# Performance work log

Measured on AMD Instinct MI355X. Metric: run time of the kernel, lower is better.

The kernel has to match this reference:

```python
import jax, jax.numpy as jnp
import numpy as np

B = 10      # number of interacting objects
NDIM = 2    # self.n: position/velocity dimensionality

# Edge list equivalent to rel_rec/rel_send one-hot matrices (edges grouped by receiver)
_rec_idx, _send_idx = np.where(~np.eye(B, dtype=bool))


def _mlp(x, W0, b0, W1, b1, W2, b2):
    # MLP with 2 hidden softplus layers, linear output
    h = jax.nn.softplus(x @ W0 + b0)
    h = jax.nn.softplus(h @ W1 + b1)
    return h @ W2 + b2


def setup_inputs() -> dict:
    key = jax.random.key(0)
    ks = jax.random.split(key, 7)
    N = 8192            # trajectories per batch
    H = 128             # hidden width of self-dynamics MLP
    Hi = 128            # hidden width of interaction MLP
    nin = 2 * NDIM      # self MLP input dim (pos+vel)
    nout = 2 * NDIM     # n_f_out for order=1
    nin_i = 3 * NDIM    # interaction MLP input dim (p1-p2, v1, v2)
    w = lambda k, shp: jax.random.normal(k, shp, jnp.float32) / np.float32(np.sqrt(shp[0]))
    return {
        "z": jax.random.normal(ks[0], (N * B, 2 * NDIM), jnp.float32),
        "fW0": w(ks[1], (nin, H)),   "fb0": jnp.zeros((H,), jnp.float32),
        "fW1": w(ks[2], (H, H)),     "fb1": jnp.zeros((H,), jnp.float32),
        "fW2": w(ks[3], (H, nout)),  "fb2": jnp.zeros((nout,), jnp.float32),
        "iW0": w(ks[4], (nin_i, Hi)),"ib0": jnp.zeros((Hi,), jnp.float32),
        "iW1": w(ks[5], (Hi, Hi)),   "ib1": jnp.zeros((Hi,), jnp.float32),
        "iW2": w(ks[6], (Hi, nout)), "ib2": jnp.zeros((nout,), jnp.float32),
    }


def reference(z, fW0, fb0, fW1, fb1, fW2, fb2, iW0, ib0, iW1, ib1, iW2, ib2):
    # One evaluation of the ODE vector field (order=1, n_aug_dyn=n_aug_st=0).
    n = NDIM
    NB = z.shape[0]
    N = NB // B
    dz_self = _mlp(z, fW0, fb0, fW1, fb1, fW2, fb2)            # [N*B, 2n]
    z3 = z.reshape(N, B, 2 * n)
    recv = z3[:, _rec_idx]                                     # [N, B(B-1), 2n] gather (node2edge)
    send = z3[:, _send_idx]
    # odefint input: (p_recv - p_send, v_recv, v_send)  -> [N, B(B-1), 3n]
    inp = jnp.concatenate([recv[..., :n] - send[..., :n], recv[..., n:], send[..., n:]], -1)
    dz_int = _mlp(inp, iW0, ib0, iW1, ib1, iW2, ib2)           # [N, B(B-1), 2n]
    dz_int = dz_int.reshape(N, B, B - 1, 2 * n).sum(2)         # sum over senders per receiver
    dz = dz_self.reshape(N, B, 2 * n) + dz_int
    return dz.reshape(NB, 2 * n)
```

## Files before the change

kernel.cpp:

```cpp
#include <hip/hip_runtime.h>
#include <hip/hip_bf16.h>

#define NDIM 2
#define BB 10
#define H 128
#define PAIRS 90
#define MROWS 128
#define LDH 136
#define USLD 132
#define LOG2E 1.4426950408889634f

typedef short short8 __attribute__((ext_vector_type(8)));
typedef float floatx4 __attribute__((ext_vector_type(4)));
typedef float floatx16 __attribute__((ext_vector_type(16)));

__device__ inline short f2bf(float x) {
    unsigned u = __float_as_uint(x);
    return (short)((u + 0x7fffu + ((u >> 16) & 1u)) >> 16);
}

#if __has_builtin(__builtin_amdgcn_cvt_pk_bf16_f32)
typedef __bf16 bf16x2_t __attribute__((ext_vector_type(2)));
__device__ inline unsigned pk2(float a, float b) {
    bf16x2_t v = __builtin_amdgcn_cvt_pk_bf16_f32(a, b);
    return __builtin_bit_cast(unsigned, v);
}
#else
__device__ inline unsigned pk2(float a, float b) {
    unsigned ua = __float_as_uint(a), ub = __float_as_uint(b);
    ua = (ua + 0x7fffu + ((ua >> 16) & 1u)) >> 16;
    ub = (ub + 0x7fffu + ((ub >> 16) & 1u)) & 0xffff0000u;
    return ua | ub;
}
#endif

__device__ inline float sp2(float xs) {
#if __has_builtin(__builtin_amdgcn_exp2f) && __has_builtin(__builtin_amdgcn_logf)
    float t = __builtin_amdgcn_exp2f(xs);
    return __builtin_amdgcn_logf(1.f + t) * 0.6931471805599453f;
#else
    return log2f(1.f + exp2f(xs)) * 0.6931471805599453f;
#endif
}

__global__ void prep_weights(const float* __restrict__ iW1, const float* __restrict__ fW1,
                             const float* __restrict__ iW2, const float* __restrict__ fW2,
                             const float* __restrict__ ib1, const float* __restrict__ fb1,
                             const float* __restrict__ iW0, const float* __restrict__ ib0,
                             const float* __restrict__ fW0, const float* __restrict__ fb0,
                             short* __restrict__ W1Fi, short* __restrict__ W1Ff,
                             short* __restrict__ W2Fi, short* __restrict__ W2Ff,
                             float* __restrict__ scal) {
    int t = blockIdx.x * blockDim.x + threadIdx.x;
    int stride = gridDim.x * blockDim.x;
    for (int fidx = t; fidx < 16384; fidx += stride) {
        int j = fidx & 7, lane = (fidx >> 3) & 63, nt = (fidx >> 9) & 3, ks = fidx >> 11;
        int k = 16 * ks + ((lane >> 5) << 3) + j;
        int n = 32 * nt + (lane & 31);
        W1Fi[fidx] = f2bf(iW1[k * H + n] * LOG2E);
        W1Ff[fidx] = f2bf(fW1[k * H + n] * LOG2E);
    }
    for (int fidx = t; fidx < 2048; fidx += stride) {
        int j = fidx & 7, lane = (fidx >> 3) & 63, ks = fidx >> 9;
        int k = 32 * ks + ((lane >> 4) << 3) + j;
        int n = lane & 15;
        W2Fi[fidx] = (n < 4) ? f2bf(iW2[k * 4 + n]) : (short)0;
        W2Ff[fidx] = (n < 4) ? f2bf(fW2[k * 4 + n]) : (short)0;
    }
    if (t < 128) {
        scal[t] = ib1[t] * LOG2E;
        scal[128 + t] = fb1[t] * LOG2E;
        scal[1024 + t] = ib0[t] * LOG2E;
        scal[1664 + t] = fb0[t] * LOG2E;
    }
    if (t < 768) scal[256 + t] = iW0[t] * LOG2E;
    if (t < 512) scal[1152 + t] = fW0[t] * LOG2E;
}

__global__ __launch_bounds__(512, 6) void fused_kernel(
    const float* __restrict__ z,
    const float* __restrict__ ib2, const float* __restrict__ fb2,
    const short* __restrict__ W1Fi, const short* __restrict__ W2Fi,
    const short* __restrict__ W1Ff, const short* __restrict__ W2Ff,
    const float* __restrict__ scal, float* __restrict__ out) {
    __shared__ __align__(16) short h0s[MROWS * LDH];
    __shared__ __align__(16) float uws[2 * BB * USLD];
    __shared__ __align__(16) float4 zs4[BB];
    float* us   = uws;
    float* wss  = uws + BB * USLD;
    float* outs = uws;

    int n = blockIdx.x;
    int tid = threadIdx.x, lane = tid & 63, wave = tid >> 6;
    int c31 = lane & 31, halfk = lane >> 5;
    int ntw = wave & 3, mhalf = wave >> 2;

    short8 af[8];
#pragma unroll
    for (int ks = 0; ks < 8; ++ks)
        af[ks] = *(const short8*)(W1Fi + ((ks * 4 + ntw) * 64 + lane) * 8);

    if (tid < BB) zs4[tid] = ((const float4*)z)[n * BB + tid];
    __syncthreads();

    {
        int c = tid & 127;
        const float* iW0s = scal + 256;
        float w0 = iW0s[c], w1 = iW0s[128 + c], w2 = iW0s[256 + c];
        float w3 = iW0s[384 + c], w4 = iW0s[512 + c], w5 = iW0s[640 + c];
        float b0v = scal[1024 + c];
        int bb0 = tid >> 7;
#pragma unroll
        for (int t = 0; t < 3; ++t) {
            int b = bb0 + 4 * t;
            if (b < BB) {
                float4 zb = zs4[b];
                us[b * USLD + c]  = b0v + zb.x * w0 + zb.y * w1 + zb.z * w2 + zb.w * w3;
                wss[b * USLD + c] = -zb.x * w0 - zb.y * w1 + zb.z * w4 + zb.w * w5;
            }
        }
    }
    if (tid < 320) {
        int b = tid >> 5, c4 = (tid & 31) * 4;
        const float* fW0s = scal + 1152;
        float4 zb = zs4[b];
        float4 q0 = *(const float4*)(fW0s + c4);
        float4 q1 = *(const float4*)(fW0s + 128 + c4);
        float4 q2 = *(const float4*)(fW0s + 256 + c4);
        float4 q3 = *(const float4*)(fW0s + 384 + c4);
        float4 qb = *(const float4*)(scal + 1664 + c4);
        float a0 = qb.x + zb.x * q0.x + zb.y * q1.x + zb.z * q2.x + zb.w * q3.x;
        float a1 = qb.y + zb.x * q0.y + zb.y * q1.y + zb.z * q2.y + zb.w * q3.y;
        float a2 = qb.z + zb.x * q0.z + zb.y * q1.z + zb.z * q2.z + zb.w * q3.z;
        float a3 = qb.w + zb.x * q0.w + zb.y * q1.w + zb.z * q2.w + zb.w * q3.w;
        uint2 pk;
        pk.x = pk2(sp2(a0), sp2(a1));
        pk.y = pk2(sp2(a2), sp2(a3));
        *(uint2*)(h0s + (96 + b) * LDH + c4) = pk;
    }
    if (tid < 352) {
        int r = 106 + (tid >> 4), kk8 = (tid & 15) * 8;
        *(uint4*)(h0s + r * LDH + kk8) = uint4{0u, 0u, 0u, 0u};
    }
    __syncthreads();

    {
        int m0 = tid >> 4, kk8 = (tid & 15) * 8;
#pragma unroll
        for (int t = 0; t < 3; ++t) {
            int m = m0 + 32 * t;
            uint4 pk = {0u, 0u, 0u, 0u};
            if (m < PAIRS) {
                int i = (m * 57) >> 9;
                int s = m - 9 * i;
                int j = s + (s >= i);
                float4 ua = *(float4*)(us + i * USLD + kk8);
                float4 ub = *(float4*)(us + i * USLD + kk8 + 4);
                float4 wa = *(float4*)(wss + j * USLD + kk8);
                float4 wb = *(float4*)(wss + j * USLD + kk8 + 4);
                pk.x = pk2(sp2(ua.x + wa.x), sp2(ua.y + wa.y));
                pk.y = pk2(sp2(ua.z + wa.z), sp2(ua.w + wa.w));
                pk.z = pk2(sp2(ub.x + wb.x), sp2(ub.y + wb.y));
                pk.w = pk2(sp2(ub.z + wb.z), sp2(ub.w + wb.w));
            }
            *(uint4*)(h0s + m * LDH + kk8) = pk;
        }
    }
    __syncthreads();

    int hb = 32 * ntw + 4 * halfk;
    floatx16 acc0, acc1;
    {
        const float* blo = scal;
        const float* bhi = mhalf ? (scal + 128) : scal;
#pragma unroll
        for (int g = 0; g < 4; ++g) {
            float4 v0 = *(const float4*)(blo + hb + 8 * g);
            float4 v1 = *(const float4*)(bhi + hb + 8 * g);
            acc0[4 * g + 0] = v0.x; acc0[4 * g + 1] = v0.y;
            acc0[4 * g + 2] = v0.z; acc0[4 * g + 3] = v0.w;
            acc1[4 * g + 0] = v1.x; acc1[4 * g + 1] = v1.y;
            acc1[4 * g + 2] = v1.z; acc1[4 * g + 3] = v1.w;
        }
    }
    int rowA = 64 * mhalf + c31;
    int rowB = rowA + 32;
#pragma unroll
    for (int ks = 0; ks < 8; ++ks) {
        short8 bf = *(const short8*)(h0s + rowA * LDH + 16 * ks + 8 * halfk);
        acc0 = __builtin_amdgcn_mfma_f32_32x32x16_bf16(af[ks], bf, acc0, 0, 0, 0);
    }
    if (mhalf) {
#pragma unroll
        for (int ks = 0; ks < 8; ++ks)
            af[ks] = *(const short8*)(W1Ff + ((ks * 4 + ntw) * 64 + lane) * 8);
    }
#pragma unroll
    for (int ks = 0; ks < 8; ++ks) {
        short8 bf = *(const short8*)(h0s + rowB * LDH + 16 * ks + 8 * halfk);
        acc1 = __builtin_amdgcn_mfma_f32_32x32x16_bf16(af[ks], bf, acc1, 0, 0, 0);
    }
    __syncthreads();

#pragma unroll
    for (int g = 0; g < 4; ++g) {
        uint2 pa, pb;
        pa.x = pk2(sp2(acc0[4 * g + 0]), sp2(acc0[4 * g + 1]));
        pa.y = pk2(sp2(acc0[4 * g + 2]), sp2(acc0[4 * g + 3]));
        pb.x = pk2(sp2(acc1[4 * g + 0]), sp2(acc1[4 * g + 1]));
        pb.y = pk2(sp2(acc1[4 * g + 2]), sp2(acc1[4 * g + 3]));
        *(uint2*)(h0s + rowA * LDH + 32 * ntw + 8 * g + 4 * halfk) = pa;
        *(uint2*)(h0s + rowB * LDH + 32 * ntw + 8 * g + 4 * halfk) = pb;
    }
    __syncthreads();

    {
        int rit = lane & 15, quad = lane >> 4;
        if (wave < 7) {
            const short* W2 = (wave == 6) ? W2Ff : W2Fi;
            const float* b2 = (wave == 6) ? fb2 : ib2;
            short8 w2v[4];
#pragma unroll
            for (int ks = 0; ks < 4; ++ks)
                w2v[ks] = *(const short8*)(W2 + (ks * 64 + lane) * 8);
            floatx4 a = {0.f, 0.f, 0.f, 0.f};
            if (quad == 0) {
                float4 bbv = *(const float4*)b2;
                a = floatx4{bbv.x, bbv.y, bbv.z, bbv.w};
            }
#pragma unroll
            for (int ks = 0; ks < 4; ++ks) {
                short8 bf = *(const short8*)(h0s + (16 * wave + rit) * LDH + 32 * ks + quad * 8);
                a = __builtin_amdgcn_mfma_f32_16x16x32_bf16(w2v[ks], bf, a, 0, 0, 0);
            }
            if (quad == 0) {
                float4 o = {a[0], a[1], a[2], a[3]};
                *(float4*)(outs + (16 * wave + rit) * 4) = o;
            }
        }
    }
    __syncthreads();

    if (tid < BB * 4) {
        int i = tid >> 2, c = tid & 3;
        float s = outs[(96 + i) * 4 + c];
#pragma unroll
        for (int p = 0; p < 9; ++p) s += outs[(9 * i + p) * 4 + c];
        out[(n * BB + i) * 4 + c] = s;
    }
}

extern "C" void kernel_launch(void* const* d_in, const int* in_sizes, int n_in,
                              void* d_out, int out_size, void* d_ws, size_t ws_size,
                              hipStream_t stream) {
    const float* z   = (const float*)d_in[0];
    const float* fW0 = (const float*)d_in[1];
    const float* fb0 = (const float*)d_in[2];
    const float* fW1 = (const float*)d_in[3];
    const float* fb1 = (const float*)d_in[4];
    const float* fW2 = (const float*)d_in[5];
    const float* fb2 = (const float*)d_in[6];
    const float* iW0 = (const float*)d_in[7];
    const float* ib0 = (const float*)d_in[8];
    const float* iW1 = (const float*)d_in[9];
    const float* ib1 = (const float*)d_in[10];
    const float* iW2 = (const float*)d_in[11];
    const float* ib2 = (const float*)d_in[12];
    float* out = (float*)d_out;

    short* wsS = (short*)d_ws;
    short* W1Fi = wsS;
    short* W1Ff = wsS + 16384;
    short* W2Fi = wsS + 32768;
    short* W2Ff = wsS + 34816;
    float* scal = (float*)(wsS + 36864);

    int NB = in_sizes[0] / (2 * NDIM);
    int Nsys = NB / BB;

    hipLaunchKernelGGL(prep_weights, dim3(128), dim3(256), 0, stream,
                       iW1, fW1, iW2, fW2, ib1, fb1, iW0, ib0, fW0, fb0,
                       W1Fi, W1Ff, W2Fi, W2Ff, scal);
    hipLaunchKernelGGL(fused_kernel, dim3(Nsys), dim3(512), 0, stream,
                       z, ib2, fb2, W1Fi, W2Fi, W1Ff, W2Ff, scal, out);
}
```

Before: 181.8 us.

## Cut registers and LDS: bf16 edge partials, polynomial softplus, streamed weight fragments

Several changes aimed at raising occupancy and trimming per-element cost. Launch bounds go from 6 to 8 waves per SIMD. Layer-1 weight fragments are streamed one k-step ahead instead of holding eight in registers, and the second-layer weights are loaded inside the loop. The per-node receiver and sender partials are stored as bf16 in LDS rather than fp32. Softplus drops the hardware log and uses max(x,0) plus a quadratic in exp(-|x|). The h0 row stride changes to 132 with split 8-byte LDS loads, presumably to reduce bank conflicts. Risks include accuracy loss from the softplus approximation and the extra bf16 rounding, and more global-load latency inside the MFMA loop.

Measured after the change: 191.0 us. 1.05x slower.

```diff
diff --git a/kernel.cpp b/kernel.cpp
--- a/kernel.cpp
+++ b/kernel.cpp
@@ -6,11 +6,13 @@
 #define H 128
 #define PAIRS 90
 #define MROWS 128
-#define LDH 136
-#define USLD 132
+#define LDH 132
+#define UST 136
 #define LOG2E 1.4426950408889634f
+#define LN2   0.6931471805599453f
 
 typedef short short8 __attribute__((ext_vector_type(8)));
+typedef short short4v __attribute__((ext_vector_type(4)));
 typedef float floatx4 __attribute__((ext_vector_type(4)));
 typedef float floatx16 __attribute__((ext_vector_type(16)));
 
@@ -35,12 +37,23 @@
 #endif
 
 __device__ inline float sp2(float xs) {
-#if __has_builtin(__builtin_amdgcn_exp2f) && __has_builtin(__builtin_amdgcn_logf)
-    float t = __builtin_amdgcn_exp2f(xs);
-    return __builtin_amdgcn_logf(1.f + t) * 0.6931471805599453f;
+    float m = fmaxf(xs, 0.f);
+#if __has_builtin(__builtin_amdgcn_exp2f)
+    float t = __builtin_amdgcn_exp2f(-fabsf(xs));
 #else
-    return log2f(1.f + exp2f(xs)) * 0.6931471805599453f;
+    float t = exp2f(-fabsf(xs));
 #endif
+    float q = fmaf(t, fmaf(t, 0.2057f, -0.6484f), 1.4426950f);
+    return fmaf(t, q, m) * LN2;
+}
+
+__device__ inline float blo(unsigned d) { return __uint_as_float(d << 16); }
+__device__ inline float bhif(unsigned d) { return __uint_as_float(d & 0xffff0000u); }
+
+__device__ inline short8 ld8(const short* p) {
+    short4v lo = *(const short4v*)p;
+    short4v hi = *(const short4v*)(p + 4);
+    return short8{lo[0], lo[1], lo[2], lo[3], hi[0], hi[1], hi[2], hi[3]};
 }
 
 __global__ void prep_weights(const float* __restrict__ iW1, const float* __restrict__ fW1,
@@ -77,47 +90,47 @@
     if (t < 512) scal[1152 + t] = fW0[t] * LOG2E;
 }
 
-__global__ __launch_bounds__(512, 6) void fused_kernel(
+__global__ __launch_bounds__(512, 8) void fused_kernel(
     const float* __restrict__ z,
     const float* __restrict__ ib2, const float* __restrict__ fb2,
     const short* __restrict__ W1Fi, const short* __restrict__ W2Fi,
     const short* __restrict__ W1Ff, const short* __restrict__ W2Ff,
     const float* __restrict__ scal, float* __restrict__ out) {
     __shared__ __align__(16) short h0s[MROWS * LDH];
-    __shared__ __align__(16) float uws[2 * BB * USLD];
+    __shared__ __align__(16) short uwsb[2 * BB * UST];
     __shared__ __align__(16) float4 zs4[BB];
-    float* us   = uws;
-    float* wss  = uws + BB * USLD;
-    float* outs = uws;
+    short* usb = uwsb;
+    short* wsb = uwsb + BB * UST;
+    float* outs = (float*)uwsb;
 
     int n = blockIdx.x;
     int tid = threadIdx.x, lane = tid & 63, wave = tid >> 6;
     int c31 = lane & 31, halfk = lane >> 5;
     int ntw = wave & 3, mhalf = wave >> 2;
 
-    short8 af[8];
-#pragma unroll
-    for (int ks = 0; ks < 8; ++ks)
-        af[ks] = *(const short8*)(W1Fi + ((ks * 4 + ntw) * 64 + lane) * 8);
-
     if (tid < BB) zs4[tid] = ((const float4*)z)[n * BB + tid];
     __syncthreads();
 
     {
-        int c = tid & 127;
         const float* iW0s = scal + 256;
-        float w0 = iW0s[c], w1 = iW0s[128 + c], w2 = iW0s[256 + c];
-        float w3 = iW0s[384 + c], w4 = iW0s[512 + c], w5 = iW0s[640 + c];
-        float b0v = scal[1024 + c];
-        int bb0 = tid >> 7;
-#pragma unroll
-        for (int t = 0; t < 3; ++t) {
-            int b = bb0 + 4 * t;
-            if (b < BB) {
-                float4 zb = zs4[b];
-                us[b * USLD + c]  = b0v + zb.x * w0 + zb.y * w1 + zb.z * w2 + zb.w * w3;
-                wss[b * USLD + c] = -zb.x * w0 - zb.y * w1 + zb.z * w4 + zb.w * w5;
-            }
+        for (int u = tid; u < 640; u += 512) {
+            int b = u >> 6, c2 = (u & 63) * 2;
+            float4 zb = zs4[b];
+            float2 p0 = *(const float2*)(iW0s + c2);
+            float2 p1 = *(const float2*)(iW0s + 128 + c2);
+            float2 p2 = *(const float2*)(iW0s + 256 + c2);
+            float2 p3 = *(const float2*)(iW0s + 384 + c2);
+            float2 p4 = *(const float2*)(iW0s + 512 + c2);
+            float2 p5 = *(const float2*)(iW0s + 640 + c2);
+            float2 pb = *(const float2*)(scal + 1024 + c2);
+            float s0 = zb.x * p0.x + zb.y * p1.x;
+            float s1 = zb.x * p0.y + zb.y * p1.y;
+            float u0 = pb.x + s0 + zb.z * p2.x + zb.w * p3.x;
+            float u1 = pb.y + s1 + zb.z * p2.y + zb.w * p3.y;
+            float w0 = -s0 + zb.z * p4.x + zb.w * p5.x;
+            float w1 = -s1 + zb.z * p4.y + zb.w * p5.y;
+            *(unsigned*)(usb + b * UST + c2) = pk2(u0, u1);
+            *(unsigned*)(wsb + b * UST + c2) = pk2(w0, w1);
         }
     }
     if (tid < 320) {
@@ -138,32 +151,35 @@
         pk.y = pk2(sp2(a2), sp2(a3));
         *(uint2*)(h0s + (96 + b) * LDH + c4) = pk;
     }
-    if (tid < 352) {
-        int r = 106 + (tid >> 4), kk8 = (tid & 15) * 8;
-        *(uint4*)(h0s + r * LDH + kk8) = uint4{0u, 0u, 0u, 0u};
-    }
-    __syncthreads();
-
-    {
-        int m0 = tid >> 4, kk8 = (tid & 15) * 8;
+    for (int t = tid; t < 726; t += 512) {
+        int r = 106 + t / 33, d2 = (t % 33) * 4;
+        *(uint2*)(h0s + r * LDH + d2) = uint2{0u, 0u};
+    }
+    __syncthreads();
+
+    {
+        int m0 = tid >> 4, c8 = (tid & 15) * 8;
 #pragma unroll
         for (int t = 0; t < 3; ++t) {
             int m = m0 + 32 * t;
-            uint4 pk = {0u, 0u, 0u, 0u};
+            uint2 o0 = {0u, 0u}, o1 = {0u, 0u};
             if (m < PAIRS) {
                 int i = (m * 57) >> 9;
                 int s = m - 9 * i;
                 int j = s + (s >= i);
-                float4 ua = *(float4*)(us + i * USLD + kk8);
-                float4 ub = *(float4*)(us + i * USLD + kk8 + 4);
-                float4 wa = *(float4*)(wss + j * USLD + kk8);
-                float4 wb = *(float4*)(wss + j * USLD + kk8 + 4);
-                pk.x = pk2(sp2(ua.x + wa.x), sp2(ua.y + wa.y));
-                pk.y = pk2(sp2(ua.z + wa.z), sp2(ua.w + wa.w));
-                pk.z = pk2(sp2(ub.x + wb.x), sp2(ub.y + wb.y));
-                pk.w = pk2(sp2(ub.z + wb.z), sp2(ub.w + wb.w));
+                uint4 uu = *(const uint4*)(usb + i * UST + c8);
+                uint4 ww = *(const uint4*)(wsb + j * UST + c8);
+                float x0 = blo(uu.x) + blo(ww.x), x1 = bhif(uu.x) + bhif(ww.x);
+                float x2 = blo(uu.y) + blo(ww.y), x3 = bhif(uu.y) + bhif(ww.y);
+                float x4 = blo(uu.z) + blo(ww.z), x5 = bhif(uu.z) + bhif(ww.z);
+                float x6 = blo(uu.w) + blo(ww.w), x7 = bhif(uu.w) + bhif(ww.w);
+                o0.x = pk2(sp2(x0), sp2(x1));
+                o0.y = pk2(sp2(x2), sp2(x3));
+                o1.x = pk2(sp2(x4), sp2(x5));
+                o1.y = pk2(sp2(x6), sp2(x7));
             }
-            *(uint4*)(h0s + m * LDH + kk8) = pk;
+            *(uint2*)(h0s + m * LDH + c8) = o0;
+            *(uint2*)(h0s + m * LDH + c8 + 4) = o1;
         }
     }
     __syncthreads();
@@ -171,12 +187,12 @@
     int hb = 32 * ntw + 4 * halfk;
     floatx16 acc0, acc1;
     {
-        const float* blo = scal;
-        const float* bhi = mhalf ? (scal + 128) : scal;
+        const float* blo_ = scal;
+        const float* bhi_ = mhalf ? (scal + 128) : scal;
 #pragma unroll
         for (int g = 0; g < 4; ++g) {
-            float4 v0 = *(const float4*)(blo + hb + 8 * g);
-            float4 v1 = *(const float4*)(bhi + hb + 8 * g);
+            float4 v0 = *(const float4*)(blo_ + hb + 8 * g);
+            float4 v1 = *(const float4*)(bhi_ + hb + 8 * g);
             acc0[4 * g + 0] = v0.x; acc0[4 * g + 1] = v0.y;
             acc0[4 * g + 2] = v0.z; acc0[4 * g + 3] = v0.w;
             acc1[4 * g + 0] = v1.x; acc1[4 * g + 1] = v1.y;
@@ -185,20 +201,29 @@
     }
     int rowA = 64 * mhalf + c31;
     int rowB = rowA + 32;
-#pragma unroll
-    for (int ks = 0; ks < 8; ++ks) {
-        short8 bf = *(const short8*)(h0s + rowA * LDH + 16 * ks + 8 * halfk);
-        acc0 = __builtin_amdgcn_mfma_f32_32x32x16_bf16(af[ks], bf, acc0, 0, 0, 0);
-    }
-    if (mhalf) {
-#pragma unroll
-        for (int ks = 0; ks < 8; ++ks)
-            af[ks] = *(const short8*)(W1Ff + ((ks * 4 + ntw) * 64 + lane) * 8);
-    }
-#pragma unroll
-    for (int ks = 0; ks < 8; ++ks) {
-        short8 bf = *(const short8*)(h0s + rowB * LDH + 16 * ks + 8 * halfk);
-        acc1 = __builtin_amdgcn_mfma_f32_32x32x16_bf16(af[ks], bf, acc1, 0, 0, 0);
+    {
+        const short* WA = W1Fi + (ntw * 64 + lane) * 8;
+        short8 a_cur = *(const short8*)WA;
+#pragma unroll
+        for (int ks = 0; ks < 8; ++ks) {
+            short8 a_nxt = a_cur;
+            if (ks < 7) a_nxt = *(const short8*)(WA + (ks + 1) * 2048);
+            short8 bf = ld8(h0s + rowA * LDH + 16 * ks + 8 * halfk);
+            acc0 = __builtin_amdgcn_mfma_f32_32x32x16_bf16(a_cur, bf, acc0, 0, 0, 0);
+            a_cur = a_nxt;
+        }
+    }
+    {
+        const short* WB = (mhalf ? W1Ff : W1Fi) + (ntw * 64 + lane) * 8;
+        short8 a_cur = *(const short8*)WB;
+#pragma unroll
+        for (int ks = 0; ks < 8; ++ks) {
+            short8 a_nxt = a_cur;
+            if (ks < 7) a_nxt = *(const short8*)(WB + (ks + 1) * 2048);
+            short8 bf = ld8(h0s + rowB * LDH + 16 * ks + 8 * halfk);
+            acc1 = __builtin_amdgcn_mfma_f32_32x32x16_bf16(a_cur, bf, acc1, 0, 0, 0);
+            a_cur = a_nxt;
+        }
     }
     __syncthreads();
 
@@ -219,10 +244,6 @@
         if (wave < 7) {
             const short* W2 = (wave == 6) ? W2Ff : W2Fi;
             const float* b2 = (wave == 6) ? fb2 : ib2;
-            short8 w2v[4];
-#pragma unroll
-            for (int ks = 0; ks < 4; ++ks)
-                w2v[ks] = *(const short8*)(W2 + (ks * 64 + lane) * 8);
             floatx4 a = {0.f, 0.f, 0.f, 0.f};
             if (quad == 0) {
                 float4 bbv = *(const float4*)b2;
@@ -230,8 +251,9 @@
             }
 #pragma unroll
             for (int ks = 0; ks < 4; ++ks) {
-                short8 bf = *(const short8*)(h0s + (16 * wave + rit) * LDH + 32 * ks + quad * 8);
-                a = __builtin_amdgcn_mfma_f32_16x16x32_bf16(w2v[ks], bf, a, 0, 0, 0);
+                short8 w2v = *(const short8*)(W2 + (ks * 64 + lane) * 8);
+                short8 bf = ld8(h0s + (16 * wave + rit) * LDH + 32 * ks + quad * 8);
+                a = __builtin_amdgcn_mfma_f32_16x16x32_bf16(w2v, bf, a, 0, 0, 0);
             }
             if (quad == 0) {
                 float4 o = {a[0], a[1], a[2], a[3]};
```
